# Kernel optimization log

Measured on AMD Instinct MI355X. Metric: run time of the kernel, lower is better.

## Reference

```python
import jax, jax.numpy as jnp
import numpy as np

D_MODEL = 512
NUM_HEADS = 8
D_HEAD = D_MODEL // NUM_HEADS


def setup_inputs() -> dict:
    key = jax.random.key(0)
    ks = jax.random.split(key, 16)
    B, S, D, H, dh = 8, 1024, D_MODEL, NUM_HEADS, D_HEAD
    s = 1.0 / np.sqrt(D)
    return {
        "query": jax.random.normal(ks[0], (B, S, D), jnp.float32),
        "key": jax.random.normal(ks[1], (B, S, D), jnp.float32),
        "value": jax.random.normal(ks[2], (B, S, D), jnp.float32),
        "pos_emb": jax.random.normal(ks[3], (B, S, D), jnp.float32),
        "Wq": jax.random.normal(ks[4], (D, D), jnp.float32) * s,
        "bq": jnp.zeros((D,), jnp.float32),
        "Wk": jax.random.normal(ks[5], (D, D), jnp.float32) * s,
        "bk": jnp.zeros((D,), jnp.float32),
        "Wv": jax.random.normal(ks[6], (D, D), jnp.float32) * s,
        "bv": jnp.zeros((D,), jnp.float32),
        "Wpos": jax.random.normal(ks[7], (D, D), jnp.float32) * s,  # pos_proj has no bias
        "Wo": jax.random.normal(ks[8], (D, D), jnp.float32) * s,
        "bo": jnp.zeros((D,), jnp.float32),
        "u_bias": jax.random.normal(ks[9], (H, dh), jnp.float32) * 0.02,
        "v_bias": jax.random.normal(ks[10], (H, dh), jnp.float32) * 0.02,
    }


def _rel_shift(x):
    # x: [B, H, S, S] -> Transformer-XL relative shift
    B, H, S1, S2 = x.shape
    x = jnp.pad(x, ((0, 0), (0, 0), (0, 0), (1, 0)))  # zero col at front
    x = x.reshape(B, H, S2 + 1, S1)[:, :, 1:, :]
    return x.reshape(B, H, S1, S2)


def reference(query, key, value, pos_emb, Wq, bq, Wk, bk, Wv, bv, Wpos, Wo, bo, u_bias, v_bias):
    B, S, D = query.shape
    H, dh = NUM_HEADS, D_HEAD
    q = (query @ Wq + bq).reshape(B, S, H, dh)      # [B,S,H,dh]
    k = (key @ Wk + bk).reshape(B, S, H, dh)
    v = (value @ Wv + bv).reshape(B, S, H, dh)
    p = (pos_emb @ Wpos).reshape(B, S, H, dh)
    content_score = jnp.einsum('bqhd,bkhd->bhqk', q + u_bias, k)
    pos_score = _rel_shift(jnp.einsum('bqhd,bkhd->bhqk', q + v_bias, p))
    score = (content_score + pos_score) / jnp.sqrt(jnp.float32(D))
    attn = jax.nn.softmax(score, axis=-1)
    ctx = jnp.einsum('bhqk,bkhd->bqhd', attn, v).reshape(B, S, D)
    return ctx @ Wo + bo
```

## Files before the change

### kernel.cpp

```cpp
#include <hip/hip_runtime.h>
#include <hip/hip_bf16.h>

typedef unsigned short u16;
typedef unsigned int u32;
typedef __attribute__((ext_vector_type(4))) float f32x4;
typedef __attribute__((ext_vector_type(8))) short s16x8;
typedef __attribute__((ext_vector_type(4))) short s16x4;

#define DEV static __device__ __forceinline__

DEV u16 f2bf(float f){ return __builtin_bit_cast(u16, __float2bfloat16(f)); }
DEV float bf2f(u16 v){ union{u32 u;float f;}x; x.u = ((u32)v)<<16; return x.f; }
DEV float bitsf(u32 u){ union{u32 u;float f;}x; x.u = u; return x.f; }

DEV f32x4 MF(s16x8 a, s16x8 b, f32x4 c){ return __builtin_amdgcn_mfma_f32_16x16x32_bf16(a,b,c,0,0,0); }

DEV s16x8 frag64(const u16* lds, int row, int slot){
  return *(const s16x8*)(lds + row*64 + ((slot ^ (row&7))<<3));
}

__global__ __launch_bounds__(256) void k_prep(
  const float* __restrict__ Wq, const float* __restrict__ Wk, const float* __restrict__ Wv,
  const float* __restrict__ Wp, const float* __restrict__ Wo, u16* __restrict__ WT)
{
  const int bx = blockIdx.x; const int mat = bx>>6, tile = bx&63;
  const float* W = (mat==0)?Wq:(mat==1)?Wk:(mat==2)?Wv:(mat==3)?Wp:Wo;
  u16* dst = WT + mat*262144;
  const int k0 = (tile>>3)<<6, n0 = (tile&7)<<6;
  __shared__ u16 L[64*68];
  const int t = threadIdx.x;
#pragma unroll
  for (int i=0;i<4;i++){
    int id = t + 256*i; int row = id>>4, c4 = (id&15)<<2;
    float4 v = *(const float4*)(W + (k0+row)*512 + n0 + c4);
    s16x4 o; o[0]=(short)f2bf(v.x); o[1]=(short)f2bf(v.y); o[2]=(short)f2bf(v.z); o[3]=(short)f2bf(v.w);
    *(s16x4*)(L + row*68 + c4) = o;
  }
  __syncthreads();
#pragma unroll
  for (int i=0;i<2;i++){
    int id = t + 256*i; int nl = id>>3, slot = id&7;
    s16x8 v;
#pragma unroll
    for (int j=0;j<8;j++) v[j] = (short)L[(slot*8+j)*68 + nl];
    *(s16x8*)(dst + (n0+nl)*512 + k0 + slot*8) = v;
  }
}

__global__ __launch_bounds__(256,2) void k_proj(
  const float* __restrict__ Xq, const float* __restrict__ Xk,
  const float* __restrict__ Xv, const float* __restrict__ Xp,
  const u16* __restrict__ WT,
  const float* __restrict__ bq, const float* __restrict__ bk, const float* __restrict__ bv,
  const float* __restrict__ ub, const float* __restrict__ vb,
  u16* __restrict__ Qu, u16* __restrict__ Qv, u16* __restrict__ Kb,
  u16* __restrict__ Pb, u16* __restrict__ Vt)
{
  const int job = blockIdx.z;
  const float* X = (job==0)?Xq:(job==1)?Xk:(job==2)?Xp:Xv;
  const int wsel = (job==0)?0:(job==1)?1:(job==2)?3:2;
  const u16* W = WT + wsel*262144;
  const int m0 = blockIdx.y*128, n0 = blockIdx.x*128;
  __shared__ u16 As[128*64];
  __shared__ u16 Bs[128*64];
  const int t = threadIdx.x, lane = t&63, w = t>>6;
  const int wm = w&1, wn = w>>1;
  f32x4 acc[4][4];
#pragma unroll
  for (int i=0;i<4;i++)
#pragma unroll
    for (int j=0;j<4;j++) acc[i][j] = (f32x4){0.f,0.f,0.f,0.f};

  for (int kt=0; kt<8; ++kt){
    const int k0 = kt*64;
    __syncthreads();
#pragma unroll
    for (int i=0;i<8;i++){
      int id = t + 256*i; int row = id>>4; int c4 = (id&15)<<2;
      float4 v = *(const float4*)(X + (m0+row)*512 + k0 + c4);
      s16x4 o; o[0]=(short)f2bf(v.x); o[1]=(short)f2bf(v.y); o[2]=(short)f2bf(v.z); o[3]=(short)f2bf(v.w);
      *(s16x4*)(As + row*64 + ((((c4>>3)^(row&7))<<3) + (c4&4))) = o;
    }
#pragma unroll
    for (int i=0;i<4;i++){
      int id = t + 256*i; int row = id>>3, slot = id&7;
      s16x8 v = *(const s16x8*)(W + (n0+row)*512 + k0 + slot*8);
      *(s16x8*)(Bs + row*64 + ((slot^(row&7))<<3)) = v;
    }
    __syncthreads();
#pragma unroll
    for (int kk=0;kk<2;kk++){
      const int slotk = kk*4 + (lane>>4);
      s16x8 xf[4], wf[4];
#pragma unroll
      for (int j=0;j<4;j++){ int r = wm*64 + j*16 + (lane&15); xf[j] = frag64(As, r, slotk); }
#pragma unroll
      for (int i=0;i<4;i++){ int r = wn*64 + i*16 + (lane&15); wf[i] = frag64(Bs, r, slotk); }
      if (job != 3){
#pragma unroll
        for (int i=0;i<4;i++)
#pragma unroll
          for (int j=0;j<4;j++) acc[i][j] = MF(wf[i], xf[j], acc[i][j]);
      } else {
#pragma unroll
        for (int i=0;i<4;i++)
#pragma unroll
          for (int j=0;j<4;j++) acc[i][j] = MF(xf[i], wf[j], acc[i][j]);
      }
    }
  }

  const int b = m0>>10;
  if (job != 3){
#pragma unroll
    for (int i=0;i<4;i++){
      const int n = n0 + wn*64 + i*16 + ((lane>>4)<<2);
      const int hh = n>>6, d = n&63;
      f32x4 b1 = {0.f,0.f,0.f,0.f}, b2 = {0.f,0.f,0.f,0.f};
      if (job==0){
        f32x4 q4 = *(const f32x4*)(bq+n); f32x4 u4 = *(const f32x4*)(ub+n); f32x4 v4 = *(const f32x4*)(vb+n);
        b1 = q4 + u4; b2 = q4 + v4;
      } else if (job==1){
        b1 = *(const f32x4*)(bk+n);
      }
#pragma unroll
      for (int j=0;j<4;j++){
        const int m = m0 + wm*64 + j*16 + (lane&15);
        const int s = m&1023;
        const int off = ((b*8+hh)*1024 + s)*64 + d;
        f32x4 a = acc[i][j];
        s16x4 o1;
#pragma unroll
        for (int r=0;r<4;r++) o1[r] = (short)f2bf(a[r]+b1[r]);
        if (job==0){
          *(s16x4*)(Qu+off) = o1;
          s16x4 o2;
#pragma unroll
          for (int r=0;r<4;r++) o2[r] = (short)f2bf(a[r]+b2[r]);
          *(s16x4*)(Qv+off) = o2;
        } else if (job==1) *(s16x4*)(Kb+off) = o1;
        else               *(s16x4*)(Pb+off) = o1;
      }
    }
  } else {
#pragma unroll
    for (int j=0;j<4;j++){
      const int n = n0 + wn*64 + j*16 + (lane&15);
      const int hh = n>>6, d = n&63;
      const float bvn = bv[n];
#pragma unroll
      for (int i=0;i<4;i++){
        const int m = m0 + wm*64 + i*16 + ((lane>>4)<<2);
        const int s = m&1023;
        f32x4 a = acc[i][j];
        s16x4 o;
#pragma unroll
        for (int r=0;r<4;r++) o[r] = (short)f2bf(a[r]+bvn);
        *(s16x4*)(Vt + ((b*8+hh)*64 + d)*1024 + s) = o;
      }
    }
  }
}

#define SC_SLOT(q, slot) ((((slot)) & ~7) | ((((slot))&7) ^ ((q)&7)))

__global__ __launch_bounds__(512,4) void k_attn(
  const u16* __restrict__ Qu, const u16* __restrict__ Qv,
  const u16* __restrict__ Kb, const u16* __restrict__ Pb,
  const u16* __restrict__ Vt, u16* __restrict__ Ctx)
{
  const int qb = blockIdx.x, h = blockIdx.y, b = blockIdx.z;
  const int q0 = qb*32;
  const int bh = b*8 + h;
  const u16* Qu_ = Qu + bh*65536;
  const u16* Qv_ = Qv + bh*65536;
  const u16* Kb_ = Kb + bh*65536;
  const u16* Pb_ = Pb + bh*65536;
  const u16* Vt_ = Vt + bh*65536;
  u16* Ctx_ = Ctx + bh*65536;
  __shared__ u16 sc[33*1024];
  __shared__ u16 Ts[64*64];
  __shared__ float stats[32];
  const int t = threadIdx.x, lane = t&63, w = t>>6;
  const int l15 = lane&15, lg = lane>>4;
  const int qband = w&1, sub = w>>1;
  const int qi = qband*16 + l15;
  const int q  = q0 + qi;
  const int srow = t>>3, sslot = t&7;
  u16* tsw = Ts + srow*64 + ((sslot^(srow&7))<<3);
  const u16* srcP = Pb_ + srow*64 + sslot*8;
  const u16* srcK = Kb_ + srow*64 + sslot*8;
  const u16* srcV = Vt_ + srow*1024 + sslot*8;

  const int priBand = w>>2, jtp = w&3;
  s16x8 qvp[2], qvb2[2];
#pragma unroll
  for (int kk=0;kk<2;kk++){
    qvp[kk]  = *(const s16x8*)(Qv_ + (q0 + priBand*16 + l15)*64 + (kk*4+lg)*8);
    int r2 = q0 + 17 + l15; if (r2 > 1023) r2 = 1023;
    qvb2[kk] = *(const s16x8*)(Qv_ + r2*64 + (kk*4+lg)*8);
  }

  {
    s16x8 p0 = *(const s16x8*)(srcP);
    s16x8 p1 = *(const s16x8*)(srcP + 4096);
    for (int u=0; u<16; ++u){
      __syncthreads();
      *(s16x8*)tsw = p0;
      p0 = p1;
      if (u+2<16) p1 = *(const s16x8*)(srcP + (u+2)*4096);
      __syncthreads();
      {
        f32x4 ps = {0.f,0.f,0.f,0.f};
#pragma unroll
        for (int kk=0;kk<2;kk++){
          s16x8 pf = frag64(Ts, jtp*16 + l15, kk*4+lg);
          ps = MF(pf, qvp[kk], ps);
        }
        const int prow = priBand*16 + l15;
        const int j0 = u*64 + jtp*16 + lg*4;
        s16x4 o;
#pragma unroll
        for (int r=0;r<4;r++) o[r] = (short)f2bf(ps[r]);
        *(s16x4*)(sc + prow*1024 + ((((j0>>2) ^ ((prow&15)<<1)))<<2)) = o;
      }
      if ((u&1) == (w>>2)){
        f32x4 ps = {0.f,0.f,0.f,0.f};
#pragma unroll
        for (int kk=0;kk<2;kk++){
          s16x8 pf = frag64(Ts, (w&3)*16 + l15, kk*4+lg);
          ps = MF(pf, qvb2[kk], ps);
        }
        if (l15 == 15){
          const int j0 = u*64 + (w&3)*16 + lg*4;
          s16x4 o;
#pragma unroll
          for (int r=0;r<4;r++) o[r] = (short)f2bf(ps[r]);
          *(s16x4*)(sc + 32*1024 + ((j0>>2)<<2)) = o;
        }
      }
    }
  }

  __syncthreads();

  u32 stash[32];
#pragma unroll
  for (int kt=0; kt<16; ++kt){
#pragma unroll
    for (int rp=0; rp<2; ++rp){
      u32 wv = 0;
#pragma unroll
      for (int hh=0; hh<2; ++hh){
        const int k = kt*64 + sub*16 + lg*4 + rp*2 + hh;
        const int above = (k > q) ? 1 : 0;
        int jj = above ? (k - q - 2) : (1023 - q + k);
        const bool zero = (k == q+1);
        if (jj < 0) jj = 0;
        const int row = qi + above;
        const int addr = row*1024 + ((((jj>>2) ^ ((row&15)<<1)))<<2) + (jj&3);
        u32 v = zero ? 0u : (u32)sc[addr];
        wv |= v << (16*hh);
      }
      stash[kt*2+rp] = wv;
    }
  }

  s16x8 qfu[2];
#pragma unroll
  for (int kk=0;kk<2;kk++)
    qfu[kk] = *(const s16x8*)(Qu_ + q*64 + (kk*4+lg)*8);

  {
    s16x8 k0r = *(const s16x8*)(srcK);
    s16x8 k1r = *(const s16x8*)(srcK + 4096);
    for (int kt=0; kt<16; ++kt){
      __syncthreads();
      *(s16x8*)tsw = k0r;
      k0r = k1r;
      if (kt+2<16) k1r = *(const s16x8*)(srcK + (kt+2)*4096);
      __syncthreads();
      f32x4 a = {0.f,0.f,0.f,0.f};
#pragma unroll
      for (int kk=0;kk<2;kk++){
        s16x8 kf = frag64(Ts, sub*16 + l15, kk*4+lg);
        a = MF(kf, qfu[kk], a);
      }
      const int kb2 = kt*64 + sub*16 + lg*4;
      const u32 w0 = stash[kt*2], w1 = stash[kt*2+1];
      const float p0 = bitsf(w0<<16), p1 = bitsf(w0 & 0xffff0000u);
      const float p2 = bitsf(w1<<16), p3 = bitsf(w1 & 0xffff0000u);
      s16x4 o;
      o[0]=(short)f2bf(a[0]+p0); o[1]=(short)f2bf(a[1]+p1);
      o[2]=(short)f2bf(a[2]+p2); o[3]=(short)f2bf(a[3]+p3);
      *(s16x4*)(sc + qi*1024 + SC_SLOT(qi, kb2>>3)*8 + (kb2&4)) = o;
    }
  }

  __syncthreads();

  {
    const int row = t>>4, c = t&15;
    float mx = -1e30f;
#pragma unroll
    for (int i=0;i<8;i++){
      const int slot = c + 16*i;
      s16x8 v = *(const s16x8*)(sc + row*1024 + SC_SLOT(row,slot)*8);
#pragma unroll
      for (int j2=0;j2<8;j2++) mx = fmaxf(mx, bf2f((u16)v[j2]));
    }
    mx = fmaxf(mx, __shfl_xor(mx,1));
    mx = fmaxf(mx, __shfl_xor(mx,2));
    mx = fmaxf(mx, __shfl_xor(mx,4));
    mx = fmaxf(mx, __shfl_xor(mx,8));
    float sum = 0.f;
    const float SCALE = 0.044194173824159216f;
#pragma unroll
    for (int i=0;i<8;i++){
      const int slot = c + 16*i;
      u16* p = sc + row*1024 + SC_SLOT(row,slot)*8;
      s16x8 v = *(const s16x8*)p;
      s16x8 o;
#pragma unroll
      for (int j2=0;j2<8;j2++){
        float e = __expf((bf2f((u16)v[j2]) - mx)*SCALE);
        sum += e; o[j2] = (short)f2bf(e);
      }
      *(s16x8*)p = o;
    }
    sum += __shfl_xor(sum,1); sum += __shfl_xor(sum,2);
    sum += __shfl_xor(sum,4); sum += __shfl_xor(sum,8);
    if (c==0) stats[row] = 1.0f/sum;
  }

  f32x4 accC = {0.f,0.f,0.f,0.f};
  {
    s16x8 v0r = *(const s16x8*)(srcV);
    s16x8 v1r = *(const s16x8*)(srcV + 64);
    for (int kt=0; kt<16; ++kt){
      __syncthreads();
      *(s16x8*)tsw = v0r;
      v0r = v1r;
      if (kt+2<16) v1r = *(const s16x8*)(srcV + (kt+2)*64);
      __syncthreads();
#pragma unroll
      for (int kk=0;kk<2;kk++){
        const int slotk = kk*4 + lg;
        s16x8 vf = frag64(Ts, sub*16 + l15, slotk);
        const int slot = kt*8 + slotk;
        s16x8 pfr = *(const s16x8*)(sc + qi*1024 + SC_SLOT(qi,slot)*8);
        accC = MF(vf, pfr, accC);
      }
    }
  }
  {
    const float inv = stats[qi];
    const int d0 = sub*16 + lg*4;
    s16x4 o;
#pragma unroll
    for (int r=0;r<4;r++) o[r] = (short)f2bf(accC[r]*inv);
    *(s16x4*)(Ctx_ + (q0+qi)*64 + d0) = o;
  }
}

__global__ __launch_bounds__(256,2) void k_out(
  const u16* __restrict__ Ctx, const u16* __restrict__ WT,
  const float* __restrict__ bo, float* __restrict__ Out)
{
  const u16* W = WT + 4*262144;
  const int m0 = blockIdx.y*128, n0 = blockIdx.x*128;
  const int b = m0>>10, s0 = m0&1023;
  __shared__ u16 As[128*64];
  __shared__ u16 Bs[128*64];
  const int t = threadIdx.x, lane = t&63, w = t>>6;
  const int wm = w&1, wn = w>>1;
  f32x4 acc[4][4];
#pragma unroll
  for (int i=0;i<4;i++)
#pragma unroll
    for (int j=0;j<4;j++) acc[i][j] = (f32x4){0.f,0.f,0.f,0.f};

  for (int kt=0; kt<8; ++kt){
    const int k0 = kt*64, hh = kt;
    __syncthreads();
#pragma unroll
    for (int i=0;i<4;i++){
      int id = t + 256*i; int row = id>>3, slot = id&7;
      s16x8 v = *(const s16x8*)(Ctx + ((b*8+hh)*1024 + s0 + row)*64 + slot*8);
      *(s16x8*)(As + row*64 + ((slot^(row&7))<<3)) = v;
    }
#pragma unroll
    for (int i=0;i<4;i++){
      int id = t + 256*i; int row = id>>3, slot = id&7;
      s16x8 v = *(const s16x8*)(W + (n0+row)*512 + k0 + slot*8);
      *(s16x8*)(Bs + row*64 + ((slot^(row&7))<<3)) = v;
    }
    __syncthreads();
#pragma unroll
    for (int kk=0;kk<2;kk++){
      const int slotk = kk*4 + (lane>>4);
      s16x8 xf[4], wf[4];
#pragma unroll
      for (int j=0;j<4;j++){ int r = wm*64 + j*16 + (lane&15); xf[j] = frag64(As, r, slotk); }
#pragma unroll
      for (int i=0;i<4;i++){ int r = wn*64 + i*16 + (lane&15); wf[i] = frag64(Bs, r, slotk); }
#pragma unroll
      for (int i=0;i<4;i++)
#pragma unroll
        for (int j=0;j<4;j++) acc[i][j] = MF(wf[i], xf[j], acc[i][j]);
    }
  }
#pragma unroll
  for (int i=0;i<4;i++){
    const int n = n0 + wn*64 + i*16 + ((lane>>4)<<2);
    f32x4 bo4 = *(const f32x4*)(bo + n);
#pragma unroll
    for (int j=0;j<4;j++){
      const int m = m0 + wm*64 + j*16 + (lane&15);
      f32x4 o = acc[i][j] + bo4;
      *(f32x4*)(Out + m*512 + n) = o;
    }
  }
}

extern "C" void kernel_launch(void* const* d_in, const int* in_sizes, int n_in,
                              void* d_out, int out_size, void* d_ws, size_t ws_size,
                              hipStream_t stream)
{
  const float* query = (const float*)d_in[0];
  const float* key   = (const float*)d_in[1];
  const float* value = (const float*)d_in[2];
  const float* pos   = (const float*)d_in[3];
  const float* Wq = (const float*)d_in[4];
  const float* bq = (const float*)d_in[5];
  const float* Wk = (const float*)d_in[6];
  const float* bk = (const float*)d_in[7];
  const float* Wv = (const float*)d_in[8];
  const float* bv = (const float*)d_in[9];
  const float* Wp = (const float*)d_in[10];
  const float* Wo = (const float*)d_in[11];
  const float* bo = (const float*)d_in[12];
  const float* ub = (const float*)d_in[13];
  const float* vb = (const float*)d_in[14];
  float* Out = (float*)d_out;

  u16* ws  = (u16*)d_ws;
  u16* WT  = ws;
  u16* Qu  = ws + 1310720;
  u16* Qv  = Qu + 4194304;
  u16* Kb  = Qv + 4194304;
  u16* Pb  = Kb + 4194304;
  u16* Vt  = Pb + 4194304;
  u16* Ctx = Vt + 4194304;

  k_prep<<<dim3(320),      dim3(256), 0, stream>>>(Wq,Wk,Wv,Wp,Wo,WT);
  k_proj<<<dim3(4,64,4),   dim3(256), 0, stream>>>(query,key,value,pos,WT,bq,bk,bv,ub,vb,Qu,Qv,Kb,Pb,Vt);
  k_attn<<<dim3(32,8,8),   dim3(512), 0, stream>>>(Qu,Qv,Kb,Pb,Vt,Ctx);
  k_out<<<dim3(4,64),      dim3(256), 0, stream>>>(Ctx,WT,bo,Out);
}
```

Baseline: 186.3 us.

## Precompute rel-shifted positional scores in a separate GEMM kernel, chunked over heads

Moves the Qv·P positional score computation out of the attention kernel into a dedicated tiled GEMM kernel. That kernel writes the relative-shifted bf16 score matrix to a global workspace, processed in four chunks of 16 batch-heads to bound workspace size. The attention kernel then streams the pre-shifted positional scores from global memory instead of recomputing them per query block with extra syncs and LDS gather. This removes redundant per-block P loads and 16 synchronized iterations. The cost is a large global round-trip of 2 MB per batch-head and eight kernel launches instead of one.

Result: slower. 229.4 us (+23.2%).

```diff
diff --git a/kernel.cpp b/kernel.cpp
--- a/kernel.cpp
+++ b/kernel.cpp
@@ -11,7 +11,6 @@
 
 DEV u16 f2bf(float f){ return __builtin_bit_cast(u16, __float2bfloat16(f)); }
 DEV float bf2f(u16 v){ union{u32 u;float f;}x; x.u = ((u32)v)<<16; return x.f; }
-DEV float bitsf(u32 u){ union{u32 u;float f;}x; x.u = u; return x.f; }
 
 DEV f32x4 MF(s16x8 a, s16x8 b, f32x4 c){ return __builtin_amdgcn_mfma_f32_16x16x32_bf16(a,b,c,0,0,0); }
 
@@ -162,23 +161,99 @@
   }
 }
 
+__global__ __launch_bounds__(256,4) void k_pos(
+  const u16* __restrict__ Qv, const u16* __restrict__ Pb,
+  u16* __restrict__ posW, int bh0)
+{
+  const int jt = blockIdx.x, qt = blockIdx.y, bhl = blockIdx.z;
+  const int bh = bh0 + bhl;
+  const int q0 = qt*128, j0 = jt*128;
+  const u16* Qv_ = Qv + bh*65536;
+  const u16* Pb_ = Pb + bh*65536;
+  u16* out = posW + bhl*1048576;
+  __shared__ u16 mem[16896];
+  u16* As = mem; u16* Bs = mem + 8192;
+  const int t = threadIdx.x, lane = t&63, w = t>>6;
+  const int l15 = lane&15, lg = lane>>4;
+
+#pragma unroll
+  for (int i=0;i<4;i++){
+    int id = t + 256*i; int row = id>>3, slot = id&7;
+    *(s16x8*)(As + row*64 + ((slot^(row&7))<<3)) = *(const s16x8*)(Qv_ + (q0+row)*64 + slot*8);
+    *(s16x8*)(Bs + row*64 + ((slot^(row&7))<<3)) = *(const s16x8*)(Pb_ + (j0+row)*64 + slot*8);
+  }
+  __syncthreads();
+
+  const int wm = w&1, wn = w>>1;
+  f32x4 acc[4][4];
+#pragma unroll
+  for (int i=0;i<4;i++)
+#pragma unroll
+    for (int j=0;j<4;j++) acc[i][j] = (f32x4){0.f,0.f,0.f,0.f};
+#pragma unroll
+  for (int kk=0;kk<2;kk++){
+    const int slotk = kk*4 + lg;
+    s16x8 qf[4], pf[4];
+#pragma unroll
+    for (int j=0;j<4;j++) qf[j] = frag64(As, wm*64 + j*16 + l15, slotk);
+#pragma unroll
+    for (int i=0;i<4;i++) pf[i] = frag64(Bs, wn*64 + i*16 + l15, slotk);
+#pragma unroll
+    for (int i=0;i<4;i++)
+#pragma unroll
+      for (int j=0;j<4;j++) acc[i][j] = MF(pf[i], qf[j], acc[i][j]);
+  }
+  __syncthreads();
+
+  u16* pst = mem;
+#pragma unroll
+  for (int i=0;i<4;i++)
+#pragma unroll
+    for (int j=0;j<4;j++){
+      const int qloc = wm*64 + j*16 + l15;
+      const int jloc = wn*64 + i*16 + lg*4;
+      s16x4 o;
+#pragma unroll
+      for (int r=0;r<4;r++) o[r] = (short)f2bf(acc[i][j][r]);
+      *(s16x4*)(pst + qloc*132 + jloc) = o;
+    }
+  __syncthreads();
+
+  for (int rr = w; rr < 129; rr += 4){
+    const int r = q0 - 1 + rr;
+    if (r < 0) continue;
+    const int base = r*1024;
+#pragma unroll
+    for (int s2=0;s2<2;s2++){
+      const int jloc = lane + s2*64;
+      if (rr >= 1){
+        const int k = jloc + j0 + r - 1023;
+        if (k >= 0) out[base + k] = pst[(rr-1)*132 + jloc];
+      }
+      if (rr <= 127){
+        const int k = jloc + j0 + r + 2;
+        if (k <= 1023) out[base + k] = pst[rr*132 + jloc];
+      }
+    }
+  }
+}
+
 #define SC_SLOT(q, slot) ((((slot)) & ~7) | ((((slot))&7) ^ ((q)&7)))
 
 __global__ __launch_bounds__(512,4) void k_attn(
-  const u16* __restrict__ Qu, const u16* __restrict__ Qv,
-  const u16* __restrict__ Kb, const u16* __restrict__ Pb,
-  const u16* __restrict__ Vt, u16* __restrict__ Ctx)
-{
-  const int qb = blockIdx.x, h = blockIdx.y, b = blockIdx.z;
+  const u16* __restrict__ Qu, const u16* __restrict__ Kb,
+  const u16* __restrict__ Vt, const u16* __restrict__ posS,
+  u16* __restrict__ Ctx, int bh0)
+{
+  const int qb = blockIdx.x, h = blockIdx.y, bz = blockIdx.z;
   const int q0 = qb*32;
-  const int bh = b*8 + h;
+  const int bhl = bz*8 + h;
+  const int bh = bh0 + bhl;
   const u16* Qu_ = Qu + bh*65536;
-  const u16* Qv_ = Qv + bh*65536;
   const u16* Kb_ = Kb + bh*65536;
-  const u16* Pb_ = Pb + bh*65536;
   const u16* Vt_ = Vt + bh*65536;
   u16* Ctx_ = Ctx + bh*65536;
-  __shared__ u16 sc[33*1024];
+  __shared__ u16 sc[32*1024];
   __shared__ u16 Ts[64*64];
   __shared__ float stats[32];
   const int t = threadIdx.x, lane = t&63, w = t>>6;
@@ -188,83 +263,9 @@
   const int q  = q0 + qi;
   const int srow = t>>3, sslot = t&7;
   u16* tsw = Ts + srow*64 + ((sslot^(srow&7))<<3);
-  const u16* srcP = Pb_ + srow*64 + sslot*8;
   const u16* srcK = Kb_ + srow*64 + sslot*8;
   const u16* srcV = Vt_ + srow*1024 + sslot*8;
-
-  const int priBand = w>>2, jtp = w&3;
-  s16x8 qvp[2], qvb2[2];
-#pragma unroll
-  for (int kk=0;kk<2;kk++){
-    qvp[kk]  = *(const s16x8*)(Qv_ + (q0 + priBand*16 + l15)*64 + (kk*4+lg)*8);
-    int r2 = q0 + 17 + l15; if (r2 > 1023) r2 = 1023;
-    qvb2[kk] = *(const s16x8*)(Qv_ + r2*64 + (kk*4+lg)*8);
-  }
-
-  {
-    s16x8 p0 = *(const s16x8*)(srcP);
-    s16x8 p1 = *(const s16x8*)(srcP + 4096);
-    for (int u=0; u<16; ++u){
-      __syncthreads();
-      *(s16x8*)tsw = p0;
-      p0 = p1;
-      if (u+2<16) p1 = *(const s16x8*)(srcP + (u+2)*4096);
-      __syncthreads();
-      {
-        f32x4 ps = {0.f,0.f,0.f,0.f};
-#pragma unroll
-        for (int kk=0;kk<2;kk++){
-          s16x8 pf = frag64(Ts, jtp*16 + l15, kk*4+lg);
-          ps = MF(pf, qvp[kk], ps);
-        }
-        const int prow = priBand*16 + l15;
-        const int j0 = u*64 + jtp*16 + lg*4;
-        s16x4 o;
-#pragma unroll
-        for (int r=0;r<4;r++) o[r] = (short)f2bf(ps[r]);
-        *(s16x4*)(sc + prow*1024 + ((((j0>>2) ^ ((prow&15)<<1)))<<2)) = o;
-      }
-      if ((u&1) == (w>>2)){
-        f32x4 ps = {0.f,0.f,0.f,0.f};
-#pragma unroll
-        for (int kk=0;kk<2;kk++){
-          s16x8 pf = frag64(Ts, (w&3)*16 + l15, kk*4+lg);
-          ps = MF(pf, qvb2[kk], ps);
-        }
-        if (l15 == 15){
-          const int j0 = u*64 + (w&3)*16 + lg*4;
-          s16x4 o;
-#pragma unroll
-          for (int r=0;r<4;r++) o[r] = (short)f2bf(ps[r]);
-          *(s16x4*)(sc + 32*1024 + ((j0>>2)<<2)) = o;
-        }
-      }
-    }
-  }
-
-  __syncthreads();
-
-  u32 stash[32];
-#pragma unroll
-  for (int kt=0; kt<16; ++kt){
-#pragma unroll
-    for (int rp=0; rp<2; ++rp){
-      u32 wv = 0;
-#pragma unroll
-      for (int hh=0; hh<2; ++hh){
-        const int k = kt*64 + sub*16 + lg*4 + rp*2 + hh;
-        const int above = (k > q) ? 1 : 0;
-        int jj = above ? (k - q - 2) : (1023 - q + k);
-        const bool zero = (k == q+1);
-        if (jj < 0) jj = 0;
-        const int row = qi + above;
-        const int addr = row*1024 + ((((jj>>2) ^ ((row&15)<<1)))<<2) + (jj&3);
-        u32 v = zero ? 0u : (u32)sc[addr];
-        wv |= v << (16*hh);
-      }
-      stash[kt*2+rp] = wv;
-    }
-  }
+  const u16* PSq  = posS + bhl*1048576 + q*1024 + sub*16 + lg*4;
 
   s16x8 qfu[2];
 #pragma unroll
@@ -274,11 +275,14 @@
   {
     s16x8 k0r = *(const s16x8*)(srcK);
     s16x8 k1r = *(const s16x8*)(srcK + 4096);
+    s16x4 pv  = *(const s16x4*)(PSq);
     for (int kt=0; kt<16; ++kt){
       __syncthreads();
       *(s16x8*)tsw = k0r;
       k0r = k1r;
       if (kt+2<16) k1r = *(const s16x8*)(srcK + (kt+2)*4096);
+      s16x4 pvn;
+      if (kt+1<16) pvn = *(const s16x4*)(PSq + (kt+1)*64);
       __syncthreads();
       f32x4 a = {0.f,0.f,0.f,0.f};
 #pragma unroll
@@ -287,13 +291,15 @@
         a = MF(kf, qfu[kk], a);
       }
       const int kb2 = kt*64 + sub*16 + lg*4;
-      const u32 w0 = stash[kt*2], w1 = stash[kt*2+1];
-      const float p0 = bitsf(w0<<16), p1 = bitsf(w0 & 0xffff0000u);
-      const float p2 = bitsf(w1<<16), p3 = bitsf(w1 & 0xffff0000u);
       s16x4 o;
-      o[0]=(short)f2bf(a[0]+p0); o[1]=(short)f2bf(a[1]+p1);
-      o[2]=(short)f2bf(a[2]+p2); o[3]=(short)f2bf(a[3]+p3);
+#pragma unroll
+      for (int r=0;r<4;r++){
+        const int k = kb2 + r;
+        const float posf = (k == q+1) ? 0.f : bf2f((u16)pv[r]);
+        o[r] = (short)f2bf(a[r] + posf);
+      }
       *(s16x4*)(sc + qi*1024 + SC_SLOT(qi, kb2>>3)*8 + (kb2&4)) = o;
+      pv = pvn;
     }
   }
 
@@ -452,9 +458,13 @@
   u16* Pb  = Kb + 4194304;
   u16* Vt  = Pb + 4194304;
   u16* Ctx = Vt + 4194304;
+  u16* posW = Ctx + 4194304;
 
   k_prep<<<dim3(320),      dim3(256), 0, stream>>>(Wq,Wk,Wv,Wp,Wo,WT);
   k_proj<<<dim3(4,64,4),   dim3(256), 0, stream>>>(query,key,value,pos,WT,bq,bk,bv,ub,vb,Qu,Qv,Kb,Pb,Vt);
-  k_attn<<<dim3(32,8,8),   dim3(512), 0, stream>>>(Qu,Qv,Kb,Pb,Vt,Ctx);
+  for (int c=0;c<4;c++){
+    k_pos <<<dim3(8,8,16), dim3(256), 0, stream>>>(Qv,Pb,posW,c*16);
+    k_attn<<<dim3(32,8,2), dim3(512), 0, stream>>>(Qu,Kb,Vt,posW,Ctx,c*16);
+  }
   k_out<<<dim3(4,64),      dim3(256), 0, stream>>>(Ctx,WT,bo,Out);
 }
```

## Double-buffer attention staging tile, remap grids for XCD locality, spill row 32

Applied to the files above, without the earlier changes.

The three K/P/V staging loops in the attention kernel now use two LDS tile buffers, which cuts each iteration to a single barrier instead of two. The extra pos-score row (row 32) moves out of LDS into a per-block global scratch buffer, which keeps shared memory within budget for the second tile. Both the projection and attention kernels switch to 1D grids whose block index maps one batch-head or row group to a single XCD, so L2 reuse of K/P/V across query blocks should improve. The cost is extra global traffic for the scratch row, two more barriers around the stats read, and reliance on round-robin XCD dispatch.

Result: no change. 185.2 us (-0.6%).

```diff
diff --git a/kernel.cpp b/kernel.cpp
--- a/kernel.cpp
+++ b/kernel.cpp
@@ -56,11 +56,14 @@
   u16* __restrict__ Qu, u16* __restrict__ Qv, u16* __restrict__ Kb,
   u16* __restrict__ Pb, u16* __restrict__ Vt)
 {
-  const int job = blockIdx.z;
+  const int Lb = blockIdx.x;
+  const int xcd = Lb & 7, li = Lb >> 3;
+  const int n0  = (li & 3) * 128;
+  const int job = (li >> 2) & 3;
+  const int m0  = (xcd*8 + (li >> 4)) * 128;
   const float* X = (job==0)?Xq:(job==1)?Xk:(job==2)?Xp:Xv;
   const int wsel = (job==0)?0:(job==1)?1:(job==2)?3:2;
   const u16* W = WT + wsel*262144;
-  const int m0 = blockIdx.y*128, n0 = blockIdx.x*128;
   __shared__ u16 As[128*64];
   __shared__ u16 Bs[128*64];
   const int t = threadIdx.x, lane = t&63, w = t>>6;
@@ -167,27 +170,31 @@
 __global__ __launch_bounds__(512,4) void k_attn(
   const u16* __restrict__ Qu, const u16* __restrict__ Qv,
   const u16* __restrict__ Kb, const u16* __restrict__ Pb,
-  const u16* __restrict__ Vt, u16* __restrict__ Ctx)
+  const u16* __restrict__ Vt, u16* __restrict__ Ctx,
+  u16* __restrict__ psR32)
 {
-  const int qb = blockIdx.x, h = blockIdx.y, b = blockIdx.z;
+  const int Lb = blockIdx.x;
+  const int xcd = Lb & 7, li = Lb >> 3;
+  const int bh = xcd*8 + (li>>5);
+  const int qb = li & 31;
   const int q0 = qb*32;
-  const int bh = b*8 + h;
   const u16* Qu_ = Qu + bh*65536;
   const u16* Qv_ = Qv + bh*65536;
   const u16* Kb_ = Kb + bh*65536;
   const u16* Pb_ = Pb + bh*65536;
   const u16* Vt_ = Vt + bh*65536;
   u16* Ctx_ = Ctx + bh*65536;
-  __shared__ u16 sc[33*1024];
-  __shared__ u16 Ts[64*64];
-  __shared__ float stats[32];
+  u16* r32 = psR32 + Lb*1024;
+  __shared__ u16 sc[32*1024];
+  __shared__ u16 Ts[2][4096];
+  float* statsF = (float*)&Ts[0][0];
   const int t = threadIdx.x, lane = t&63, w = t>>6;
   const int l15 = lane&15, lg = lane>>4;
   const int qband = w&1, sub = w>>1;
   const int qi = qband*16 + l15;
   const int q  = q0 + qi;
   const int srow = t>>3, sslot = t&7;
-  u16* tsw = Ts + srow*64 + ((sslot^(srow&7))<<3);
+  const int tso = srow*64 + ((sslot^(srow&7))<<3);
   const u16* srcP = Pb_ + srow*64 + sslot*8;
   const u16* srcK = Kb_ + srow*64 + sslot*8;
   const u16* srcV = Vt_ + srow*1024 + sslot*8;
@@ -202,19 +209,19 @@
   }
 
   {
-    s16x8 p0 = *(const s16x8*)(srcP);
-    s16x8 p1 = *(const s16x8*)(srcP + 4096);
+    s16x8 rc = *(const s16x8*)(srcP);
+    s16x8 rn = *(const s16x8*)(srcP + 4096);
     for (int u=0; u<16; ++u){
+      *(s16x8*)(&Ts[u&1][0] + tso) = rc;
+      rc = rn;
+      if (u+2<16) rn = *(const s16x8*)(srcP + (u+2)*4096);
       __syncthreads();
-      *(s16x8*)tsw = p0;
-      p0 = p1;
-      if (u+2<16) p1 = *(const s16x8*)(srcP + (u+2)*4096);
-      __syncthreads();
+      const u16* Tsc = &Ts[u&1][0];
       {
         f32x4 ps = {0.f,0.f,0.f,0.f};
 #pragma unroll
         for (int kk=0;kk<2;kk++){
-          s16x8 pf = frag64(Ts, jtp*16 + l15, kk*4+lg);
+          s16x8 pf = frag64(Tsc, jtp*16 + l15, kk*4+lg);
           ps = MF(pf, qvp[kk], ps);
         }
         const int prow = priBand*16 + l15;
@@ -228,7 +235,7 @@
         f32x4 ps = {0.f,0.f,0.f,0.f};
 #pragma unroll
         for (int kk=0;kk<2;kk++){
-          s16x8 pf = frag64(Ts, (w&3)*16 + l15, kk*4+lg);
+          s16x8 pf = frag64(Tsc, (w&3)*16 + l15, kk*4+lg);
           ps = MF(pf, qvb2[kk], ps);
         }
         if (l15 == 15){
@@ -236,7 +243,7 @@
           s16x4 o;
 #pragma unroll
           for (int r=0;r<4;r++) o[r] = (short)f2bf(ps[r]);
-          *(s16x4*)(sc + 32*1024 + ((j0>>2)<<2)) = o;
+          *(s16x4*)(r32 + j0) = o;
         }
       }
     }
@@ -258,8 +265,13 @@
         const bool zero = (k == q+1);
         if (jj < 0) jj = 0;
         const int row = qi + above;
-        const int addr = row*1024 + ((((jj>>2) ^ ((row&15)<<1)))<<2) + (jj&3);
-        u32 v = zero ? 0u : (u32)sc[addr];
+        u32 v;
+        if (row >= 32)      v = (u32)r32[jj];
+        else {
+          const int addr = row*1024 + ((((jj>>2) ^ ((row&15)<<1)))<<2) + (jj&3);
+          v = (u32)sc[addr];
+        }
+        if (zero) v = 0u;
         wv |= v << (16*hh);
       }
       stash[kt*2+rp] = wv;
@@ -272,18 +284,18 @@
     qfu[kk] = *(const s16x8*)(Qu_ + q*64 + (kk*4+lg)*8);
 
   {
-    s16x8 k0r = *(const s16x8*)(srcK);
-    s16x8 k1r = *(const s16x8*)(srcK + 4096);
+    s16x8 rc = *(const s16x8*)(srcK);
+    s16x8 rn = *(const s16x8*)(srcK + 4096);
     for (int kt=0; kt<16; ++kt){
+      *(s16x8*)(&Ts[kt&1][0] + tso) = rc;
+      rc = rn;
+      if (kt+2<16) rn = *(const s16x8*)(srcK + (kt+2)*4096);
       __syncthreads();
-      *(s16x8*)tsw = k0r;
-      k0r = k1r;
-      if (kt+2<16) k1r = *(const s16x8*)(srcK + (kt+2)*4096);
-      __syncthreads();
+      const u16* Tsc = &Ts[kt&1][0];
       f32x4 a = {0.f,0.f,0.f,0.f};
 #pragma unroll
       for (int kk=0;kk<2;kk++){
-        s16x8 kf = frag64(Ts, sub*16 + l15, kk*4+lg);
+        s16x8 kf = frag64(Tsc, sub*16 + l15, kk*4+lg);
         a = MF(kf, qfu[kk], a);
       }
       const int kb2 = kt*64 + sub*16 + lg*4;
@@ -330,23 +342,27 @@
     }
     sum += __shfl_xor(sum,1); sum += __shfl_xor(sum,2);
     sum += __shfl_xor(sum,4); sum += __shfl_xor(sum,8);
-    if (c==0) stats[row] = 1.0f/sum;
-  }
+    if (c==0) statsF[row] = 1.0f/sum;
+  }
+
+  __syncthreads();
+  const float inv = statsF[qi];
+  __syncthreads();
 
   f32x4 accC = {0.f,0.f,0.f,0.f};
   {
-    s16x8 v0r = *(const s16x8*)(srcV);
-    s16x8 v1r = *(const s16x8*)(srcV + 64);
+    s16x8 rc = *(const s16x8*)(srcV);
+    s16x8 rn = *(const s16x8*)(srcV + 64);
     for (int kt=0; kt<16; ++kt){
+      *(s16x8*)(&Ts[kt&1][0] + tso) = rc;
+      rc = rn;
+      if (kt+2<16) rn = *(const s16x8*)(srcV + (kt+2)*64);
       __syncthreads();
-      *(s16x8*)tsw = v0r;
-      v0r = v1r;
-      if (kt+2<16) v1r = *(const s16x8*)(srcV + (kt+2)*64);
-      __syncthreads();
+      const u16* Tsc = &Ts[kt&1][0];
 #pragma unroll
       for (int kk=0;kk<2;kk++){
         const int slotk = kk*4 + lg;
-        s16x8 vf = frag64(Ts, sub*16 + l15, slotk);
+        s16x8 vf = frag64(Tsc, sub*16 + l15, slotk);
         const int slot = kt*8 + slotk;
         s16x8 pfr = *(const s16x8*)(sc + qi*1024 + SC_SLOT(qi,slot)*8);
         accC = MF(vf, pfr, accC);
@@ -354,7 +370,6 @@
     }
   }
   {
-    const float inv = stats[qi];
     const int d0 = sub*16 + lg*4;
     s16x4 o;
 #pragma unroll
@@ -452,9 +467,10 @@
   u16* Pb  = Kb + 4194304;
   u16* Vt  = Pb + 4194304;
   u16* Ctx = Vt + 4194304;
-
-  k_prep<<<dim3(320),      dim3(256), 0, stream>>>(Wq,Wk,Wv,Wp,Wo,WT);
-  k_proj<<<dim3(4,64,4),   dim3(256), 0, stream>>>(query,key,value,pos,WT,bq,bk,bv,ub,vb,Qu,Qv,Kb,Pb,Vt);
-  k_attn<<<dim3(32,8,8),   dim3(512), 0, stream>>>(Qu,Qv,Kb,Pb,Vt,Ctx);
-  k_out<<<dim3(4,64),      dim3(256), 0, stream>>>(Ctx,WT,bo,Out);
-}
+  u16* psR32 = Ctx + 4194304;
+
+  k_prep<<<dim3(320),  dim3(256), 0, stream>>>(Wq,Wk,Wv,Wp,Wo,WT);
+  k_proj<<<dim3(1024), dim3(256), 0, stream>>>(query,key,value,pos,WT,bq,bk,bv,ub,vb,Qu,Qv,Kb,Pb,Vt);
+  k_attn<<<dim3(2048), dim3(512), 0, stream>>>(Qu,Qv,Kb,Pb,Vt,Ctx,psR32);
+  k_out<<<dim3(4,64),  dim3(256), 0, stream>>>(Ctx,WT,bo,Out);
+}
```
